# Performance work log

Measured on AMD Instinct MI355X. Metric: run time of the kernel, lower is better.

The kernel has to match this reference:

```python
import jax, jax.numpy as jnp
import numpy as np

B, N, HID, HEADS, LAYERS, POOL = 2, 2048, 256, 4, 2, 128
D = HID // HEADS  # per-head dim


def attn_pool(x, w1, b1, w2, b2):
    # x: [B,N,HID]; mask is all-ones in this module's forward, so plain softmax
    s = jnp.tanh(x @ w1 + b1) @ w2 + b2            # [B,N]
    a = jax.nn.softmax(s, axis=-1)                  # [B,N]
    return jnp.einsum('bn,bnc->bc', a, x)           # [B,HID]


def gat_layer(x, adj_mask, proj_w, a_src, a_dst):
    # x: [B,N,HID] -> h: [B,N,HEADS,D]
    h = (x @ proj_w).reshape(x.shape[0], x.shape[1], HEADS, D)
    src = jnp.einsum('bnhd,hd->bnh', h, a_src)      # [B,N,H]
    dst = jnp.einsum('bnhd,hd->bnh', h, a_dst)      # [B,N,H]
    logits = src[:, :, None, :] + dst[:, None, :, :]  # [B,i,j,H]
    logits = jnp.where(logits >= 0, logits, 0.2 * logits)  # leaky_relu(0.2)
    logits = jnp.where(adj_mask[..., None], logits, jnp.float32(-1e9))
    attn = jax.nn.softmax(logits, axis=2)           # softmax over j (neighbors)
    out = jnp.einsum('bijh,bjhd->bihd', attn, h)
    return out.reshape(x.shape[0], x.shape[1], HEADS * D)


def setup_inputs() -> dict:
    key = jax.random.key(0)
    ks = jax.random.split(key, 16)
    sd = 0.05
    gene_expr = jax.random.normal(ks[0], (B, N), dtype=jnp.float32)
    gene_adj = jax.random.randint(ks[1], (B, N, N), 0, 2, dtype=jnp.int32)
    in_w = jax.random.normal(ks[2], (HID,), dtype=jnp.float32) * sd
    in_b = jax.random.normal(ks[3], (HID,), dtype=jnp.float32) * sd
    proj_w = jax.random.normal(ks[4], (LAYERS, HID, HID), dtype=jnp.float32) * sd
    attn_src = jax.random.normal(ks[5], (LAYERS, HEADS, D), dtype=jnp.float32) * sd
    attn_dst = jax.random.normal(ks[6], (LAYERS, HEADS, D), dtype=jnp.float32) * sd
    pool_w1 = jax.random.normal(ks[7], (LAYERS, HID, POOL), dtype=jnp.float32) * sd
    pool_b1 = jax.random.normal(ks[8], (LAYERS, POOL), dtype=jnp.float32) * sd
    pool_w2 = jax.random.normal(ks[9], (LAYERS, POOL), dtype=jnp.float32) * sd
    pool_b2 = jax.random.normal(ks[10], (LAYERS,), dtype=jnp.float32) * sd
    ip_w1 = jax.random.normal(ks[11], (HID, POOL), dtype=jnp.float32) * sd
    ip_b1 = jax.random.normal(ks[12], (POOL,), dtype=jnp.float32) * sd
    ip_w2 = jax.random.normal(ks[13], (POOL,), dtype=jnp.float32) * sd
    ip_b2 = jax.random.normal(ks[14], (), dtype=jnp.float32) * sd
    return dict(gene_expr=gene_expr, gene_adj=gene_adj, in_w=in_w, in_b=in_b,
                proj_w=proj_w, attn_src=attn_src, attn_dst=attn_dst,
                pool_w1=pool_w1, pool_b1=pool_b1, pool_w2=pool_w2, pool_b2=pool_b2,
                ip_w1=ip_w1, ip_b1=ip_b1, ip_w2=ip_w2, ip_b2=ip_b2)


def reference(gene_expr, gene_adj, in_w, in_b, proj_w, attn_src, attn_dst,
              pool_w1, pool_b1, pool_w2, pool_b2, ip_w1, ip_b1, ip_w2, ip_b2):
    # input_proj: Linear(1, HID) on gene_expr[...,None], then relu
    x = jax.nn.relu(gene_expr[:, :, None] * in_w + in_b)  # [B,N,HID]
    raw_pooled = attn_pool(x, ip_w1, ip_b1, ip_w2, ip_b2)
    adj_mask = gene_adj > 0
    node_outs, pooled_outs = [], []
    cur = x
    for l in range(LAYERS):
        cur = gat_layer(cur, adj_mask, proj_w[l], attn_src[l], attn_dst[l])
        cur = jax.nn.elu(cur)
        node_outs.append(cur)
        pooled_outs.append(attn_pool(cur, pool_w1[l], pool_b1[l], pool_w2[l], pool_b2[l]))
    # (raw_pooled, node_out_0, node_out_1, pooled_0, pooled_1); final_pooled == pooled_outs[-1]
    return (raw_pooled, *node_outs, *pooled_outs)
```

## Files before the change

kernel.cpp:

```cpp
#include <hip/hip_runtime.h>
#include <hip/hip_bf16.h>

#define B_ 2
#define N_ 2048
#define HID_ 256
#define HEADS_ 4
#define D_ 64
#define POOL_ 128

typedef __bf16 bf16;
typedef __bf16 bf16x8 __attribute__((ext_vector_type(8)));
typedef float f32x4 __attribute__((ext_vector_type(4)));

__device__ __forceinline__ float fast_tanh(float x) {
    x = fminf(fmaxf(x, -15.f), 15.f);
    float t = __expf(2.f * x);
    return (t - 1.f) / (t + 1.f);
}

__global__ void k_setup(const int* __restrict__ adj, unsigned* __restrict__ am,
                        const float* __restrict__ ge, const float* __restrict__ iw,
                        const float* __restrict__ ib, bf16* __restrict__ xb,
                        const float* __restrict__ proj_w, const float* __restrict__ ipw1,
                        const float* __restrict__ pw1, bf16* __restrict__ wT0,
                        bf16* __restrict__ wT1, bf16* __restrict__ ipw1T,
                        bf16* __restrict__ w1T0, bf16* __restrict__ w1T1) {
    int blk = blockIdx.x, tid = threadIdx.x;
    if (blk < 32768) {
        int gid = blk * 256 + tid;
        int v = adj[gid];
        unsigned long long mask = __ballot(v > 0);
        int lane = tid & 63;
        if (lane == 0) am[gid >> 5] = (unsigned)mask;
        else if (lane == 32) am[gid >> 5] = (unsigned)(mask >> 32);
    } else if (blk < 36864) {
        int row = blk - 32768;
        float g = ge[row];
        float v = fmaxf(g * iw[tid] + ib[tid], 0.f);
        xb[row * HID_ + tid] = (bf16)v;
    } else {
        int o = (blk - 36864) * 256 + tid;
        const float* src; bf16* dst; int Nc, loc;
        if (o < 65536)       { src = proj_w;         dst = wT0;   Nc = 256; loc = o; }
        else if (o < 131072) { src = proj_w + 65536; dst = wT1;   Nc = 256; loc = o - 65536; }
        else if (o < 163840) { src = ipw1;           dst = ipw1T; Nc = 128; loc = o - 131072; }
        else if (o < 196608) { src = pw1;            dst = w1T0;  Nc = 128; loc = o - 163840; }
        else                 { src = pw1 + 32768;    dst = w1T1;  Nc = 128; loc = o - 196608; }
        int n = loc >> 8, k = loc & 255;
        dst[loc] = (bf16)src[k * Nc + n];
    }
}

__device__ __forceinline__ void pool_sw_body(const bf16* __restrict__ A,
                                             const bf16* __restrict__ W1T,
                                             const float* __restrict__ b1,
                                             const float* __restrict__ w2,
                                             const float* __restrict__ b2,
                                             float* __restrict__ part,
                                             float* __restrict__ pz,
                                             int slot, int b, int ch, char* smemraw) {
    int n0 = ch * 16;
    int tid = threadIdx.x;
    int w = tid >> 6, lane = tid & 63, r = lane & 15, g = lane >> 4;
    const bf16* ap = A + ((long long)(b * N_ + n0) + r) * 256 + g * 8;
    f32x4 acc[2] = {{0,0,0,0},{0,0,0,0}};
    for (int ks = 0; ks < 256; ks += 32) {
        bf16x8 af = *(const bf16x8*)(ap + ks);
        #pragma unroll
        for (int nf = 0; nf < 2; ++nf) {
            bf16x8 bfr = *(const bf16x8*)(W1T + (w * 32 + nf * 16 + r) * 256 + ks + g * 8);
            acc[nf] = __builtin_amdgcn_mfma_f32_16x16x32_bf16(af, bfr, acc[nf], 0, 0, 0);
        }
    }
    float b1v[2], w2v[2];
    #pragma unroll
    for (int nf = 0; nf < 2; ++nf) {
        b1v[nf] = b1[w * 32 + nf * 16 + r];
        w2v[nf] = w2[w * 32 + nf * 16 + r];
    }
    float (*pred)[16] = (float (*)[16])smemraw;
    float* el = (float*)(smemraw + 256);
    #pragma unroll
    for (int q = 0; q < 4; ++q) {
        float p = fast_tanh(acc[0][q] + b1v[0]) * w2v[0] + fast_tanh(acc[1][q] + b1v[1]) * w2v[1];
        p += __shfl_xor(p, 1); p += __shfl_xor(p, 2);
        p += __shfl_xor(p, 4); p += __shfl_xor(p, 8);
        if (r == 0) pred[w][g * 4 + q] = p;
    }
    __syncthreads();
    if (tid < 16) {
        float s = pred[0][tid] + pred[1][tid] + pred[2][tid] + pred[3][tid] + b2[0];
        el[tid] = __expf(s);
    }
    __syncthreads();
    if (tid == 0) {
        float z = 0.f;
        #pragma unroll
        for (int n = 0; n < 16; ++n) z += el[n];
        pz[(slot * B_ + b) * 128 + ch] = z;
    }
    const bf16* xp = A + (long long)(b * N_ + n0) * 256 + tid;
    float accum = 0.f;
    #pragma unroll
    for (int n = 0; n < 16; ++n) accum += el[n] * (float)xp[n * 256];
    part[(((long long)slot * B_ + b) * 128 + ch) * 256 + tid] = accum;
}

__global__ __launch_bounds__(256) void k_gemm_h_pool(const bf16* __restrict__ A,
                                                     const bf16* __restrict__ WT,
                                                     const float* __restrict__ as,
                                                     const float* __restrict__ ad,
                                                     bf16* __restrict__ hbT,
                                                     float* __restrict__ srcM,
                                                     float* __restrict__ dstT,
                                                     const bf16* __restrict__ W1T,
                                                     const float* __restrict__ b1,
                                                     const float* __restrict__ w2,
                                                     const float* __restrict__ b2,
                                                     float* __restrict__ part,
                                                     float* __restrict__ pz, int slot) {
    __shared__ __align__(16) char smem[16640];
    int blk = blockIdx.x;
    if (blk >= 256) {
        int pb = blk - 256;
        pool_sw_body(A, W1T, b1, w2, b2, part, pz, slot, pb >> 7, pb & 127, smem);
        return;
    }
    int i0 = (blk & 63) * 64, hd = blk >> 6;
    int n0 = hd * 64;
    int w = threadIdx.x >> 6, lane = threadIdx.x & 63, r = lane & 15, g = lane >> 4;
    const bf16* ap = A + (i0 + w * 16 + r) * 256 + g * 8;
    f32x4 acc[4] = {{0,0,0,0},{0,0,0,0},{0,0,0,0},{0,0,0,0}};
    for (int ks = 0; ks < 256; ks += 32) {
        bf16x8 af = *(const bf16x8*)(ap + ks);
        #pragma unroll
        for (int nf = 0; nf < 4; ++nf) {
            bf16x8 bfr = *(const bf16x8*)(WT + (n0 + nf * 16 + r) * 256 + ks + g * 8);
            acc[nf] = __builtin_amdgcn_mfma_f32_16x16x32_bf16(af, bfr, acc[nf], 0, 0, 0);
        }
    }
    int b = i0 >> 11, nbase = i0 & 2047;
    int bh = b * HEADS_ + hd;
    float asv[4], adv[4];
    #pragma unroll
    for (int nf = 0; nf < 4; ++nf) {
        asv[nf] = as[hd * 64 + nf * 16 + r];
        adv[nf] = ad[hd * 64 + nf * 16 + r];
    }
    float (*tr)[65] = (float (*)[65])smem;
    #pragma unroll
    for (int q = 0; q < 4; ++q) {
        int ln = w * 16 + g * 4 + q;
        float ps = 0.f, pd = 0.f;
        #pragma unroll
        for (int nf = 0; nf < 4; ++nf) {
            float v = acc[nf][q];
            ps += v * asv[nf];
            pd += v * adv[nf];
            tr[nf * 16 + r][ln] = v;
        }
        ps += __shfl_xor(ps, 1); ps += __shfl_xor(ps, 2);
        ps += __shfl_xor(ps, 4); ps += __shfl_xor(ps, 8);
        pd += __shfl_xor(pd, 1); pd += __shfl_xor(pd, 2);
        pd += __shfl_xor(pd, 4); pd += __shfl_xor(pd, 8);
        if (r == 0) {
            srcM[bh * N_ + nbase + ln] = ps;
            dstT[bh * N_ + nbase + ln] = pd;
        }
    }
    __syncthreads();
    int ld = threadIdx.x >> 2, ln0 = (threadIdx.x & 3) * 16;
    bf16x8 o0, o1;
    #pragma unroll
    for (int e = 0; e < 8; ++e) {
        o0[e] = (bf16)tr[ld][ln0 + e];
        o1[e] = (bf16)tr[ld][ln0 + 8 + e];
    }
    bf16* hp = hbT + ((long long)bh * D_ + ld) * N_ + nbase + ln0;
    *(bf16x8*)(hp) = o0;
    *(bf16x8*)(hp + 8) = o1;
}

__global__ __launch_bounds__(256) void k_pool_sw(const bf16* __restrict__ A,
                                                 const bf16* __restrict__ W1T,
                                                 const float* __restrict__ b1,
                                                 const float* __restrict__ w2,
                                                 const float* __restrict__ b2,
                                                 float* __restrict__ part,
                                                 float* __restrict__ pz, int slot) {
    __shared__ __align__(16) char smem[320];
    pool_sw_body(A, W1T, b1, w2, b2, part, pz, slot, blockIdx.y, blockIdx.x, smem);
}

__global__ __launch_bounds__(512, 4) void k_attn(const float* __restrict__ srcM,
                                                 const float* __restrict__ dstT,
                                                 const unsigned* __restrict__ am,
                                                 const bf16* __restrict__ hbT,
                                                 float* __restrict__ nodeOut,
                                                 bf16* __restrict__ xbNext) {
    int it = blockIdx.x, hd = blockIdx.y, b = blockIdx.z;
    int i0 = it * 32;
    int tid = threadIdx.x;
    int w = tid >> 6, lane = tid & 63, r = lane & 15, g = lane >> 4;
    int rg = w >> 2, wj = w & 3;
    int bh = b * HEADS_ + hd;
    const float* drow = dstT + bh * N_;
    const bf16* vbase = hbT + (long long)bh * D_ * N_;

    __shared__ __align__(16) char smem[34816];
    bf16* vt = (bf16*)smem;
    float (*accs)[16][68] = (float (*)[16][68])smem;
    __shared__ float lred[8][16];

    int i = i0 + rg * 16 + r;
    const unsigned* mrow = am + ((long long)(b * N_ + i)) * 64;
    float sv = srcM[bh * N_ + i];

    f32x4 acc[4] = {{0,0,0,0},{0,0,0,0},{0,0,0,0},{0,0,0,0}};
    float l = 0.f;

    bf16x8 st[4];
    #pragma unroll
    for (int k = 0; k < 4; ++k) {
        int s = tid + k * 512, d = s >> 5, seg = s & 31;
        st[k] = *(const bf16x8*)(vbase + d * N_ + seg * 8);
    }

    #pragma unroll
    for (int t = 0; t < 8; ++t) {
        #pragma unroll
        for (int k = 0; k < 4; ++k) {
            int s = tid + k * 512, d = s >> 5, seg = s & 31;
            *(bf16x8*)(vt + d * 264 + seg * 8) = st[k];
        }
        __syncthreads();
        if (t < 7) {
            #pragma unroll
            for (int k = 0; k < 4; ++k) {
                int s = tid + k * 512, d = s >> 5, seg = s & 31;
                st[k] = *(const bf16x8*)(vbase + d * N_ + (t + 1) * 256 + seg * 8);
            }
        }
        #pragma unroll
        for (int s = 0; s < 2; ++s) {
            int jb = t * 256 + wj * 64 + s * 32 + g * 8;
            float4 dv0 = *(const float4*)(drow + jb);
            float4 dv1 = *(const float4*)(drow + jb + 4);
            unsigned mb = (mrow[t * 8 + wj * 2 + s] >> (g * 8)) & 0xFFu;
            float dd[8] = {dv0.x, dv0.y, dv0.z, dv0.w, dv1.x, dv1.y, dv1.z, dv1.w};
            bf16x8 af;
            float es[8];
            #pragma unroll
            for (int tt = 0; tt < 8; ++tt) {
                float s2 = sv + dd[tt];
                float lv = fmaxf(s2, 0.2f * s2);
                float e2 = __expf(lv);
                e2 = ((mb >> tt) & 1u) ? e2 : 0.f;
                es[tt] = e2;
                af[tt] = (bf16)e2;
            }
            l += ((es[0] + es[1]) + (es[2] + es[3])) + ((es[4] + es[5]) + (es[6] + es[7]));
            #pragma unroll
            for (int nf = 0; nf < 4; ++nf) {
                bf16x8 vf = *(const bf16x8*)(vt + (nf * 16 + r) * 264 + wj * 64 + s * 32 + g * 8);
                acc[nf] = __builtin_amdgcn_mfma_f32_16x16x32_bf16(af, vf, acc[nf], 0, 0, 0);
            }
        }
        __syncthreads();
    }

    l += __shfl_xor(l, 16);
    l += __shfl_xor(l, 32);
    if (g == 0) lred[w][r] = l;
    #pragma unroll
    for (int nf = 0; nf < 4; ++nf)
        #pragma unroll
        for (int q = 0; q < 4; ++q)
            accs[w][g * 4 + q][nf * 16 + r] = acc[nf][q];
    __syncthreads();

    int cc = lane;
    #pragma unroll
    for (int k = 0; k < 4; ++k) {
        int rr = w * 4 + k;
        int rg2 = rr >> 4, rl = rr & 15;
        float ls = 0.f, v = 0.f;
        #pragma unroll
        for (int w2 = 0; w2 < 4; ++w2) {
            ls += lred[rg2 * 4 + w2][rl];
            v += accs[rg2 * 4 + w2][rl][cc];
        }
        v /= ls;
        float o = v > 0.f ? v : expm1f(v);
        int idx = (b * N_ + i0 + rr) * HID_ + hd * D_ + cc;
        nodeOut[idx] = o;
        xbNext[idx] = (bf16)o;
    }
}

__global__ __launch_bounds__(256) void k_pool_finals(const float* __restrict__ part,
                                                     const float* __restrict__ pz,
                                                     float* __restrict__ outRaw,
                                                     float* __restrict__ pool0,
                                                     float* __restrict__ pool1) {
    int slot = blockIdx.x >> 1, b = blockIdx.x & 1;
    int tid = threadIdx.x;
    int lane = tid & 63, w = tid >> 6;
    float z = (tid < 128) ? pz[(slot * B_ + b) * 128 + tid] : 0.f;
    #pragma unroll
    for (int o = 1; o < 64; o <<= 1) z += __shfl_xor(z, o);
    __shared__ float red[4];
    if (lane == 0) red[w] = z;
    __syncthreads();
    float Z = red[0] + red[1] + red[2] + red[3];
    float acc = 0.f;
    #pragma unroll 8
    for (int ch = 0; ch < 128; ++ch)
        acc += part[(((long long)slot * B_ + b) * 128 + ch) * 256 + tid];
    float* out = slot == 0 ? outRaw : (slot == 1 ? pool0 : pool1);
    out[b * HID_ + tid] = acc / Z;
}

extern "C" void kernel_launch(void* const* d_in, const int* in_sizes, int n_in,
                              void* d_out, int out_size, void* d_ws, size_t ws_size,
                              hipStream_t stream) {
    const float* ge     = (const float*)d_in[0];
    const int*   adj    = (const int*)d_in[1];
    const float* in_w   = (const float*)d_in[2];
    const float* in_b   = (const float*)d_in[3];
    const float* proj_w = (const float*)d_in[4];
    const float* a_src  = (const float*)d_in[5];
    const float* a_dst  = (const float*)d_in[6];
    const float* pw1    = (const float*)d_in[7];
    const float* pb1    = (const float*)d_in[8];
    const float* pw2    = (const float*)d_in[9];
    const float* pb2    = (const float*)d_in[10];
    const float* ipw1   = (const float*)d_in[11];
    const float* ipb1   = (const float*)d_in[12];
    const float* ipw2   = (const float*)d_in[13];
    const float* ipb2   = (const float*)d_in[14];

    char* ws = (char*)d_ws;
    bf16*     xb    = (bf16*)(ws + 0);
    bf16*     hbT   = (bf16*)(ws + 2097152);
    float*    srcM  = (float*)(ws + 4194304);
    float*    dstT  = (float*)(ws + 4259840);
    unsigned* am    = (unsigned*)(ws + 4325376);
    bf16*     wT0   = (bf16*)(ws + 5373952);
    bf16*     wT1   = wT0 + 65536;
    bf16*     ipw1T = wT1 + 65536;
    bf16*     w1T0  = ipw1T + 32768;
    bf16*     w1T1  = w1T0 + 32768;
    float*    part  = (float*)(ws + 5832704);
    float*    pz    = (float*)(ws + 6619136);

    float* outRaw = (float*)d_out;
    float* node0  = outRaw + 512;
    float* node1  = node0 + 1048576;
    float* pool0  = node1 + 1048576;
    float* pool1  = pool0 + 512;

    k_setup<<<37760, 256, 0, stream>>>(adj, am, ge, in_w, in_b, xb,
                                       proj_w, ipw1, pw1, wT0, wT1, ipw1T, w1T0, w1T1);

    k_gemm_h_pool<<<512, 256, 0, stream>>>(xb, wT0, a_src, a_dst, hbT, srcM, dstT,
                                           ipw1T, ipb1, ipw2, ipb2, part, pz, 0);
    k_attn<<<dim3(64, 4, 2), 512, 0, stream>>>(srcM, dstT, am, hbT, node0, xb);

    k_gemm_h_pool<<<512, 256, 0, stream>>>(xb, wT1, a_src + 256, a_dst + 256, hbT, srcM, dstT,
                                           w1T0, pb1, pw2, pb2, part, pz, 1);
    k_attn<<<dim3(64, 4, 2), 512, 0, stream>>>(srcM, dstT, am, hbT, node1, xb);

    k_pool_sw<<<dim3(128, B_), 256, 0, stream>>>(xb, w1T1, pb1 + POOL_, pw2 + 1, pb2 + 1,
                                                 part, pz, 2);
    k_pool_finals<<<6, 256, 0, stream>>>(part, pz, outRaw, pool0, pool1);
}
```

Before: 105.1 us.

## Fold adjacency bitmask into gemm launch and pool finals into attention launch

Moves the adjacency-to-bitmask conversion out of the setup kernel into extra blocks of the first projection GEMM launch. It also computes the raw and layer-0 pooled outputs inside extra blocks of the second attention kernel, leaving a small final kernel for the last pool. The aim is to overlap the memory-bound mask build with GEMM work and cut launch and tail overhead. Log2e is folded into the attention vectors so the softmax uses exp2 instead of exp. In exchange, the launches are heterogeneous and the gemm launch carries a large grid.

```diff
diff --git a/kernel.cpp b/kernel.cpp
--- a/kernel.cpp
+++ b/kernel.cpp
@@ -7,6 +7,7 @@
 #define HEADS_ 4
 #define D_ 64
 #define POOL_ 128
+#define LOG2E_ 1.4426950408889634f
 
 typedef __bf16 bf16;
 typedef __bf16 bf16x8 __attribute__((ext_vector_type(8)));
@@ -18,28 +19,19 @@
     return (t - 1.f) / (t + 1.f);
 }
 
-__global__ void k_setup(const int* __restrict__ adj, unsigned* __restrict__ am,
-                        const float* __restrict__ ge, const float* __restrict__ iw,
+__global__ void k_setup(const float* __restrict__ ge, const float* __restrict__ iw,
                         const float* __restrict__ ib, bf16* __restrict__ xb,
                         const float* __restrict__ proj_w, const float* __restrict__ ipw1,
                         const float* __restrict__ pw1, bf16* __restrict__ wT0,
                         bf16* __restrict__ wT1, bf16* __restrict__ ipw1T,
                         bf16* __restrict__ w1T0, bf16* __restrict__ w1T1) {
     int blk = blockIdx.x, tid = threadIdx.x;
-    if (blk < 32768) {
-        int gid = blk * 256 + tid;
-        int v = adj[gid];
-        unsigned long long mask = __ballot(v > 0);
-        int lane = tid & 63;
-        if (lane == 0) am[gid >> 5] = (unsigned)mask;
-        else if (lane == 32) am[gid >> 5] = (unsigned)(mask >> 32);
-    } else if (blk < 36864) {
-        int row = blk - 32768;
-        float g = ge[row];
+    if (blk < 4096) {
+        float g = ge[blk];
         float v = fmaxf(g * iw[tid] + ib[tid], 0.f);
-        xb[row * HID_ + tid] = (bf16)v;
+        xb[blk * HID_ + tid] = (bf16)v;
     } else {
-        int o = (blk - 36864) * 256 + tid;
+        int o = (blk - 4096) * 256 + tid;
         const float* src; bf16* dst; int Nc, loc;
         if (o < 65536)       { src = proj_w;         dst = wT0;   Nc = 256; loc = o; }
         else if (o < 131072) { src = proj_w + 65536; dst = wT1;   Nc = 256; loc = o - 65536; }
@@ -118,9 +110,21 @@
                                                      const float* __restrict__ w2,
                                                      const float* __restrict__ b2,
                                                      float* __restrict__ part,
-                                                     float* __restrict__ pz, int slot) {
+                                                     float* __restrict__ pz, int slot,
+                                                     const int* __restrict__ adj,
+                                                     unsigned* __restrict__ am) {
     __shared__ __align__(16) char smem[16640];
     int blk = blockIdx.x;
+    int tid = threadIdx.x;
+    if (blk >= 512) {
+        int gid = (blk - 512) * 256 + tid;
+        int v = adj[gid];
+        unsigned long long mask = __ballot(v > 0);
+        int lane = tid & 63;
+        if (lane == 0) am[gid >> 5] = (unsigned)mask;
+        else if (lane == 32) am[gid >> 5] = (unsigned)(mask >> 32);
+        return;
+    }
     if (blk >= 256) {
         int pb = blk - 256;
         pool_sw_body(A, W1T, b1, w2, b2, part, pz, slot, pb >> 7, pb & 127, smem);
@@ -128,7 +132,7 @@
     }
     int i0 = (blk & 63) * 64, hd = blk >> 6;
     int n0 = hd * 64;
-    int w = threadIdx.x >> 6, lane = threadIdx.x & 63, r = lane & 15, g = lane >> 4;
+    int w = tid >> 6, lane = tid & 63, r = lane & 15, g = lane >> 4;
     const bf16* ap = A + (i0 + w * 16 + r) * 256 + g * 8;
     f32x4 acc[4] = {{0,0,0,0},{0,0,0,0},{0,0,0,0},{0,0,0,0}};
     for (int ks = 0; ks < 256; ks += 32) {
@@ -144,8 +148,8 @@
     float asv[4], adv[4];
     #pragma unroll
     for (int nf = 0; nf < 4; ++nf) {
-        asv[nf] = as[hd * 64 + nf * 16 + r];
-        adv[nf] = ad[hd * 64 + nf * 16 + r];
+        asv[nf] = as[hd * 64 + nf * 16 + r] * LOG2E_;
+        adv[nf] = ad[hd * 64 + nf * 16 + r] * LOG2E_;
     }
     float (*tr)[65] = (float (*)[65])smem;
     #pragma unroll
@@ -169,7 +173,7 @@
         }
     }
     __syncthreads();
-    int ld = threadIdx.x >> 2, ln0 = (threadIdx.x & 3) * 16;
+    int ld = tid >> 2, ln0 = (tid & 3) * 16;
     bf16x8 o0, o1;
     #pragma unroll
     for (int e = 0; e < 8; ++e) {
@@ -192,13 +196,54 @@
     pool_sw_body(A, W1T, b1, w2, b2, part, pz, slot, blockIdx.y, blockIdx.x, smem);
 }
 
+__device__ __forceinline__ void pool_final512(const float* __restrict__ part,
+                                              const float* __restrict__ pz,
+                                              float* __restrict__ outRaw,
+                                              float* __restrict__ pool0,
+                                              int idx2, char* smemraw) {
+    int slot = idx2 >> 1, b = idx2 & 1;
+    int tid = threadIdx.x, lane = tid & 63, w = tid >> 6;
+    float* red = (float*)smemraw;
+    float (*pr)[256] = (float (*)[256])(smemraw + 64);
+    float z = (tid < 128) ? pz[(slot * B_ + b) * 128 + tid] : 0.f;
+    #pragma unroll
+    for (int o = 1; o < 64; o <<= 1) z += __shfl_xor(z, o);
+    if (lane == 0) red[w] = z;
+    __syncthreads();
+    float Z = red[0] + red[1];
+    int c = tid & 255, half = tid >> 8;
+    float acc = 0.f;
+    #pragma unroll 8
+    for (int k = 0; k < 64; ++k) {
+        int ch = half * 64 + k;
+        acc += part[(((long long)slot * B_ + b) * 128 + ch) * 256 + c];
+    }
+    pr[half][c] = acc;
+    __syncthreads();
+    if (tid < 256) {
+        float* out = slot == 0 ? outRaw : pool0;
+        out[b * HID_ + tid] = (pr[0][tid] + pr[1][tid]) / Z;
+    }
+}
+
 __global__ __launch_bounds__(512, 4) void k_attn(const float* __restrict__ srcM,
                                                  const float* __restrict__ dstT,
                                                  const unsigned* __restrict__ am,
                                                  const bf16* __restrict__ hbT,
                                                  float* __restrict__ nodeOut,
-                                                 bf16* __restrict__ xbNext) {
-    int it = blockIdx.x, hd = blockIdx.y, b = blockIdx.z;
+                                                 bf16* __restrict__ xbNext,
+                                                 const float* __restrict__ part,
+                                                 const float* __restrict__ pz,
+                                                 float* __restrict__ outRaw,
+                                                 float* __restrict__ pool0) {
+    __shared__ __align__(16) char smem[34816];
+    __shared__ float lred[8][16];
+    int blk = blockIdx.x;
+    if (blk >= 512) {
+        pool_final512(part, pz, outRaw, pool0, blk - 512, smem);
+        return;
+    }
+    int it = blk & 63, hd = (blk >> 6) & 3, b = blk >> 8;
     int i0 = it * 32;
     int tid = threadIdx.x;
     int w = tid >> 6, lane = tid & 63, r = lane & 15, g = lane >> 4;
@@ -207,10 +252,8 @@
     const float* drow = dstT + bh * N_;
     const bf16* vbase = hbT + (long long)bh * D_ * N_;
 
-    __shared__ __align__(16) char smem[34816];
     bf16* vt = (bf16*)smem;
     float (*accs)[16][68] = (float (*)[16][68])smem;
-    __shared__ float lred[8][16];
 
     int i = i0 + rg * 16 + r;
     const unsigned* mrow = am + ((long long)(b * N_ + i)) * 64;
@@ -254,7 +297,7 @@
             for (int tt = 0; tt < 8; ++tt) {
                 float s2 = sv + dd[tt];
                 float lv = fmaxf(s2, 0.2f * s2);
-                float e2 = __expf(lv);
+                float e2 = exp2f(lv);
                 e2 = ((mb >> tt) & 1u) ? e2 : 0.f;
                 es[tt] = e2;
                 af[tt] = (bf16)e2;
@@ -298,15 +341,13 @@
     }
 }
 
-__global__ __launch_bounds__(256) void k_pool_finals(const float* __restrict__ part,
+__global__ __launch_bounds__(256) void k_pool_final2(const float* __restrict__ part,
                                                      const float* __restrict__ pz,
-                                                     float* __restrict__ outRaw,
-                                                     float* __restrict__ pool0,
                                                      float* __restrict__ pool1) {
-    int slot = blockIdx.x >> 1, b = blockIdx.x & 1;
+    int b = blockIdx.x;
     int tid = threadIdx.x;
     int lane = tid & 63, w = tid >> 6;
-    float z = (tid < 128) ? pz[(slot * B_ + b) * 128 + tid] : 0.f;
+    float z = (tid < 128) ? pz[(2 * B_ + b) * 128 + tid] : 0.f;
     #pragma unroll
     for (int o = 1; o < 64; o <<= 1) z += __shfl_xor(z, o);
     __shared__ float red[4];
@@ -316,9 +357,8 @@
     float acc = 0.f;
     #pragma unroll 8
     for (int ch = 0; ch < 128; ++ch)
-        acc += part[(((long long)slot * B_ + b) * 128 + ch) * 256 + tid];
-    float* out = slot == 0 ? outRaw : (slot == 1 ? pool0 : pool1);
-    out[b * HID_ + tid] = acc / Z;
+        acc += part[(((long long)2 * B_ + b) * 128 + ch) * 256 + tid];
+    pool1[b * HID_ + tid] = acc / Z;
 }
 
 extern "C" void kernel_launch(void* const* d_in, const int* in_sizes, int n_in,
@@ -360,18 +400,22 @@
     float* pool0  = node1 + 1048576;
     float* pool1  = pool0 + 512;
 
-    k_setup<<<37760, 256, 0, stream>>>(adj, am, ge, in_w, in_b, xb,
-                                       proj_w, ipw1, pw1, wT0, wT1, ipw1T, w1T0, w1T1);
-
-    k_gemm_h_pool<<<512, 256, 0, stream>>>(xb, wT0, a_src, a_dst, hbT, srcM, dstT,
-                                           ipw1T, ipb1, ipw2, ipb2, part, pz, 0);
-    k_attn<<<dim3(64, 4, 2), 512, 0, stream>>>(srcM, dstT, am, hbT, node0, xb);
+    k_setup<<<4992, 256, 0, stream>>>(ge, in_w, in_b, xb,
+                                      proj_w, ipw1, pw1, wT0, wT1, ipw1T, w1T0, w1T1);
+
+    k_gemm_h_pool<<<33280, 256, 0, stream>>>(xb, wT0, a_src, a_dst, hbT, srcM, dstT,
+                                             ipw1T, ipb1, ipw2, ipb2, part, pz, 0,
+                                             adj, am);
+    k_attn<<<512, 512, 0, stream>>>(srcM, dstT, am, hbT, node0, xb,
+                                    part, pz, outRaw, pool0);
 
     k_gemm_h_pool<<<512, 256, 0, stream>>>(xb, wT1, a_src + 256, a_dst + 256, hbT, srcM, dstT,
-                                           w1T0, pb1, pw2, pb2, part, pz, 1);
-    k_attn<<<dim3(64, 4, 2), 512, 0, stream>>>(srcM, dstT, am, hbT, node1, xb);
+                                           w1T0, pb1, pw2, pb2, part, pz, 1,
+                                           adj, am);
+    k_attn<<<516, 512, 0, stream>>>(srcM, dstT, am, hbT, node1, xb,
+                                    part, pz, outRaw, pool0);
 
     k_pool_sw<<<dim3(128, B_), 256, 0, stream>>>(xb, w1T1, pb1 + POOL_, pw2 + 1, pb2 + 1,
                                                  part, pz, 2);
-    k_pool_finals<<<6, 256, 0, stream>>>(part, pz, outRaw, pool0, pool1);
-}
+    k_pool_final2<<<B_, 256, 0, stream>>>(part, pz, pool1);
+}
```

Result: slower. 112.3 us (+6.8%).
